# Kernel tuning notes

Hardware: AMD Instinct MI355X
Metric: run time of the kernel (lower is better)

## Reference

```python
import jax, jax.numpy as jnp
import numpy as np

N_NODES = 32768
N_EDGES = 65536
NODE_IN = 4
EDGE_IN = 4
HIDDEN = 64
LN_EPS = 1e-5


def setup_inputs() -> dict:
    key = jax.random.key(0)
    ks = jax.random.split(key, 20)
    s = 0.05
    inp = {
        "x": jax.random.normal(ks[0], (N_NODES, NODE_IN), dtype=jnp.float32),
        "edge_attr": jax.random.normal(ks[1], (N_EDGES, EDGE_IN), dtype=jnp.float32),
        "edge_index": jax.random.randint(ks[2], (2, N_EDGES), 0, N_NODES, dtype=jnp.int64),
        "batch": jnp.zeros((N_NODES,), dtype=jnp.int64),
        # layer 1: edge MLP edge_in->64->node_in*hidden, root [node_in,hidden]
        "e1_w1": jax.random.normal(ks[3], (EDGE_IN, 64), dtype=jnp.float32) * s,
        "e1_b1": jnp.zeros((64,), jnp.float32),
        "e1_w2": jax.random.normal(ks[4], (64, NODE_IN * HIDDEN), dtype=jnp.float32) * s,
        "e1_b2": jnp.zeros((NODE_IN * HIDDEN,), jnp.float32),
        "root1": jax.random.normal(ks[5], (NODE_IN, HIDDEN), dtype=jnp.float32) * s,
        "bias1": jnp.zeros((HIDDEN,), jnp.float32),
        "ln1_g": jnp.ones((HIDDEN,), jnp.float32),
        "ln1_b": jnp.zeros((HIDDEN,), jnp.float32),
        # layer 2: edge MLP edge_in->128->hidden*hidden, root [hidden,hidden]
        "e2_w1": jax.random.normal(ks[6], (EDGE_IN, 128), dtype=jnp.float32) * s,
        "e2_b1": jnp.zeros((128,), jnp.float32),
        "e2_w2": jax.random.normal(ks[7], (128, HIDDEN * HIDDEN), dtype=jnp.float32) * s,
        "e2_b2": jnp.zeros((HIDDEN * HIDDEN,), jnp.float32),
        "root2": jax.random.normal(ks[8], (HIDDEN, HIDDEN), dtype=jnp.float32) * s,
        "bias2": jnp.zeros((HIDDEN,), jnp.float32),
        "ln2_g": jnp.ones((HIDDEN,), jnp.float32),
        "ln2_b": jnp.zeros((HIDDEN,), jnp.float32),
    }
    return inp


def _nnconv(x, src, dst, edge_attr, ew1, eb1, ew2, eb2, root, bias, n_nodes):
    # edge-conditioned weights: [E, in_ch, out_ch]
    in_ch = x.shape[1]
    out_ch = root.shape[1]
    h = jax.nn.relu(edge_attr @ ew1 + eb1) @ ew2 + eb2
    W = h.reshape(-1, in_ch, out_ch)
    # gather source features, per-edge matvec, scatter-mean to dest
    msg = jnp.einsum('ei,eio->eo', x[src], W)  # [E, out_ch]
    summed = jax.ops.segment_sum(msg, dst, num_segments=n_nodes)
    cnt = jax.ops.segment_sum(jnp.ones((dst.shape[0],), msg.dtype), dst,
                              num_segments=n_nodes)
    agg = summed / jnp.maximum(cnt, 1.0)[:, None]
    return agg + x @ root + bias


def _layernorm(x, g, b):
    m = x.mean(-1, keepdims=True)
    v = ((x - m) ** 2).mean(-1, keepdims=True)
    return (x - m) * jax.lax.rsqrt(v + LN_EPS) * g + b


def reference(x, edge_attr, e1_w1, e1_b1, e1_w2, e1_b2, root1, bias1, ln1_g, ln1_b,
              e2_w1, e2_b1, e2_w2, e2_b2, root2, bias2, ln2_g, ln2_b,
              edge_index, batch):
    src, dst = edge_index[0], edge_index[1]
    n = x.shape[0]
    h = _nnconv(x, src, dst, edge_attr, e1_w1, e1_b1, e1_w2, e1_b2, root1, bias1, n)
    h = _layernorm(jax.nn.relu(h), ln1_g, ln1_b)  # dropout = identity (eval)
    h = _nnconv(h, src, dst, edge_attr, e2_w1, e2_b1, e2_w2, e2_b2, root2, bias2, n)
    h = _layernorm(jax.nn.relu(h), ln2_g, ln2_b)
    # global mean pool (single graph -> [1, hidden])
    gs = jax.ops.segment_sum(h, batch, num_segments=1)
    gc = jax.ops.segment_sum(jnp.ones((n,), h.dtype), batch, num_segments=1)
    return gs / jnp.maximum(gc, 1.0)[:, None]
```

## Files before the change

kernel.cpp:

```cpp
#include <hip/hip_runtime.h>

#define N_NODES 32768
#define N_EDGES 65536

typedef float f32x4 __attribute__((ext_vector_type(4)));
typedef short s16x8 __attribute__((ext_vector_type(8)));

__device__ __forceinline__ unsigned short f2bf(float f){
  unsigned u = __float_as_uint(f);
  u += 0x7FFFu + ((u >> 16) & 1u);
  return (unsigned short)(u >> 16);
}
__device__ __forceinline__ float bf2f(unsigned short b){
  return __uint_as_float(((unsigned)b) << 16);
}

__global__ void k_zero(int* __restrict__ p, int n){
  int i = blockIdx.x * 256 + threadIdx.x;
  if (i < n) p[i] = 0;
}

__global__ void k_prep(const float* __restrict__ e2_w2, const float* __restrict__ e2_b2,
                       const float* __restrict__ e1_w2,
                       unsigned short* __restrict__ W2f, unsigned short* __restrict__ T1g){
  int idx = blockIdx.x * 256 + threadIdx.x;
  if (idx < 129 * 4096){
    int j = idx & 7, l = (idx >> 3) & 63, half = (idx >> 9) & 1, ot = (idx >> 10) & 3, kf = idx >> 12;
    int i = half * 32 + ((l >> 4) << 3) + j;
    int o = ot * 16 + (l & 15);
    float v = (kf < 128) ? e2_w2[kf * 4096 + i * 64 + o] : e2_b2[i * 64 + o];
    W2f[idx] = f2bf(v);
  } else if (idx < 129 * 4096 + 16384){
    int t = idx - 129 * 4096;
    int j = t & 7, l = (t >> 3) & 63, half = (t >> 9) & 1, ot = (t >> 10) & 3, i = t >> 12;
    int kf = half * 32 + ((l >> 4) << 3) + j;
    int o = ot * 16 + (l & 15);
    T1g[t] = f2bf(e1_w2[kf * 256 + i * 64 + o]);
  }
}

__global__ void k_hist(const int* __restrict__ ei, int* __restrict__ cnti){
  int i = blockIdx.x * 256 + threadIdx.x;
  if (i < N_EDGES) atomicAdd(cnti + ei[N_EDGES + i], 1);
}

__global__ void k_scanA(const int* __restrict__ cnti, int* __restrict__ lex, int* __restrict__ bsum){
  const int tid = threadIdx.x;
  int n = blockIdx.x * 256 + tid;
  int c = cnti[n];
  int v = c;
  int lane = tid & 63;
  #pragma unroll
  for (int d = 1; d < 64; d <<= 1){
    int t = __shfl_up(v, d);
    if (lane >= d) v += t;
  }
  __shared__ int wsum[4];
  if (lane == 63) wsum[tid >> 6] = v;
  __syncthreads();
  int off = 0;
  for (int i = 0; i < (tid >> 6); ++i) off += wsum[i];
  lex[n] = off + v - c;
  if (tid == 255) bsum[blockIdx.x] = off + v;
}

__global__ void k_scanB(const int* __restrict__ bsum, int* __restrict__ bsx){
  const int tid = threadIdx.x;
  int c = bsum[tid];
  int v = c;
  int lane = tid & 63;
  #pragma unroll
  for (int d = 1; d < 64; d <<= 1){
    int t = __shfl_up(v, d);
    if (lane >= d) v += t;
  }
  __shared__ int w0;
  if (tid == 63) w0 = v;
  __syncthreads();
  if (tid >= 64) v += w0;
  bsx[tid] = v - c;
}

__global__ void k_fill(const int* __restrict__ ei, const int* __restrict__ lex,
                       const int* __restrict__ bsx, int* __restrict__ cur,
                       int* __restrict__ eslot){
  int e = blockIdx.x * 256 + threadIdx.x;
  if (e < N_EDGES){
    int d = ei[N_EDGES + e];
    int base = lex[d] + bsx[d >> 8];
    eslot[e] = base + atomicAdd(cur + d, 1);
  }
}

__launch_bounds__(256, 4)
__global__ void k_msg1(const float* __restrict__ x, const float* __restrict__ ea,
                       const int* __restrict__ ei, const int* __restrict__ eslot,
                       const float* __restrict__ e1_w1, const float* __restrict__ e1_b1,
                       const float* __restrict__ e1_b2,
                       const unsigned short* __restrict__ T1g,
                       float* __restrict__ msg)
{
  __shared__ float eas[64 * 4];
  __shared__ unsigned short F1f[8 * 64 * 8];
  const int tid = threadIdx.x;
  const int eblk = blockIdx.x * 64;

  if (tid < 64) ((float4*)eas)[tid] = ((const float4*)ea)[eblk + tid];
  __syncthreads();
  {
    int kf = tid & 63, eh = tid >> 6;
    float w0 = e1_w1[kf], w1 = e1_w1[64 + kf], w2 = e1_w1[128 + kf], w3 = e1_w1[192 + kf];
    float bb = e1_b1[kf];
    int half = kf >> 5, hi = (kf >> 3) & 3, j = kf & 7;
    for (int e = eh * 16; e < eh * 16 + 16; ++e){
      float s = fmaf(eas[e*4+0], w0, fmaf(eas[e*4+1], w1, fmaf(eas[e*4+2], w2, fmaf(eas[e*4+3], w3, bb))));
      F1f[(((e >> 4) * 2 + half) * 64 + hi * 16 + (e & 15)) * 8 + j] = f2bf(fmaxf(s, 0.f));
    }
  }
  __syncthreads();

  const int l = tid & 63, lm = l & 15, lg = l >> 4;
  const int ot = tid >> 6;
  int esl[4];
  float xs[4][4];
  s16x8 bf[4][2];
  #pragma unroll
  for (int et = 0; et < 4; ++et){
    int e = eblk + et * 16 + lm;
    int s = ei[e];
    esl[et] = eslot[e];
    float4 xv = *(const float4*)(x + s * 4);
    xs[et][0] = xv.x; xs[et][1] = xv.y; xs[et][2] = xv.z; xs[et][3] = xv.w;
    bf[et][0] = ((const s16x8*)F1f)[(et * 2 + 0) * 64 + l];
    bf[et][1] = ((const s16x8*)F1f)[(et * 2 + 1) * 64 + l];
  }
  f32x4 acc[4];
  #pragma unroll
  for (int et = 0; et < 4; ++et) acc[et] = (f32x4){0.f, 0.f, 0.f, 0.f};

  #pragma unroll
  for (int i = 0; i < 4; ++i){
    const s16x8* p = (const s16x8*)(T1g + (i * 4 + ot) * 1024);
    s16x8 a0 = p[l], a1 = p[64 + l];
    #pragma unroll
    for (int et = 0; et < 4; ++et){
      f32x4 g = (f32x4){0.f, 0.f, 0.f, 0.f};
      g = __builtin_amdgcn_mfma_f32_16x16x32_bf16(a0, bf[et][0], g, 0, 0, 0);
      g = __builtin_amdgcn_mfma_f32_16x16x32_bf16(a1, bf[et][1], g, 0, 0, 0);
      acc[et] += xs[et][i] * g;
    }
  }
  float b2v[4][4];
  #pragma unroll
  for (int i = 0; i < 4; ++i)
    #pragma unroll
    for (int r = 0; r < 4; ++r) b2v[i][r] = e1_b2[i * 64 + ot * 16 + lg * 4 + r];
  #pragma unroll
  for (int et = 0; et < 4; ++et)
    #pragma unroll
    for (int r = 0; r < 4; ++r)
      #pragma unroll
      for (int i = 0; i < 4; ++i) acc[et][r] = fmaf(xs[et][i], b2v[i][r], acc[et][r]);

  #pragma unroll
  for (int et = 0; et < 4; ++et)
    *(f32x4*)(msg + (size_t)esl[et] * 64 + ot * 16 + lg * 4) = acc[et];
}

__launch_bounds__(256)
__global__ void k_node1(const float* __restrict__ x, const float* __restrict__ root1,
                        const float* __restrict__ bias1, const float* __restrict__ lng,
                        const float* __restrict__ lnb, const int* __restrict__ cnti,
                        const int* __restrict__ lex, const int* __restrict__ bsx,
                        const float* __restrict__ msg, unsigned short* __restrict__ h1b)
{
  const int tid = threadIdx.x;
  int n = blockIdx.x * 4 + (tid >> 6);
  int o = tid & 63;
  int rp = lex[n] + bsx[n >> 8];
  int deg = cnti[n];
  float s = 0.f;
  for (int j = 0; j < deg; ++j) s += msg[(size_t)(rp + j) * 64 + o];
  float v = s * (1.f / fmaxf((float)deg, 1.f));
  float4 xv = *(const float4*)(x + n * 4);
  v = fmaf(xv.x, root1[o], v);
  v = fmaf(xv.y, root1[64 + o], v);
  v = fmaf(xv.z, root1[128 + o], v);
  v = fmaf(xv.w, root1[192 + o], v);
  v = fmaxf(v + bias1[o], 0.f);
  float m = v;
  #pragma unroll
  for (int d = 32; d > 0; d >>= 1) m += __shfl_xor(m, d);
  m *= (1.f / 64.f);
  float dd = v - m;
  float var = dd * dd;
  #pragma unroll
  for (int d = 32; d > 0; d >>= 1) var += __shfl_xor(var, d);
  var *= (1.f / 64.f);
  float out = dd * rsqrtf(var + 1e-5f) * lng[o] + lnb[o];
  h1b[n * 64 + o] = f2bf(out);
}

__launch_bounds__(512, 4)
__global__ void k_msg2(const float* __restrict__ ea, const int* __restrict__ ei,
                       const int* __restrict__ eslot,
                       const float* __restrict__ e2_w1, const float* __restrict__ e2_b1,
                       const unsigned short* __restrict__ h1b,
                       const unsigned short* __restrict__ W2f,
                       float* __restrict__ msg)
{
  __shared__ float eas[128 * 4];
  __shared__ float F2s[128 * 132];
  const int tid = threadIdx.x;
  const int eblk = blockIdx.x * 128;
  if (tid < 128) ((float4*)eas)[tid] = ((const float4*)ea)[eblk + tid];
  __syncthreads();
  {
    int kf = tid & 127, q = tid >> 7;
    float w0 = e2_w1[kf], w1 = e2_w1[128 + kf], w2 = e2_w1[256 + kf], w3 = e2_w1[384 + kf];
    float bb = e2_b1[kf];
    for (int e = q * 32; e < q * 32 + 32; ++e){
      float s = fmaf(eas[e*4+0], w0, fmaf(eas[e*4+1], w1, fmaf(eas[e*4+2], w2, fmaf(eas[e*4+3], w3, bb))));
      F2s[e * 132 + kf] = fmaxf(s, 0.f);
    }
  }
  __syncthreads();

  const int w = tid >> 6, l = tid & 63, lm = l & 15, lg = l >> 4;
  const int ot = w >> 1, eh = w & 1;
  int f2base[4], esl[4];
  s16x8 bh[4][2];
  #pragma unroll
  for (int et = 0; et < 4; ++et){
    int eloc = eh * 64 + et * 16 + lm;
    int e = eblk + eloc;
    int s = ei[e];
    esl[et] = eslot[e];
    f2base[et] = eloc * 132;
    const s16x8* hp = (const s16x8*)(h1b + s * 64);
    bh[et][0] = hp[lg];
    bh[et][1] = hp[4 + lg];
  }
  f32x4 acc[4];
  #pragma unroll
  for (int et = 0; et < 4; ++et) acc[et] = (f32x4){0.f, 0.f, 0.f, 0.f};

  const unsigned short* wbase = W2f + ot * 1024;
  s16x8 A0[2], A1[2], A2[2], A3[2];
  #define LOADA(DST, KF) { const s16x8* p = (const s16x8*)(wbase + (size_t)(KF) * 4096); DST[0] = p[l]; DST[1] = p[64 + l]; }
  #define STEP(A, J) { \
    _Pragma("unroll") \
    for (int et = 0; et < 4; ++et){ \
      float f2v = f2c[et][J]; \
      f32x4 g = (f32x4){0.f, 0.f, 0.f, 0.f}; \
      g = __builtin_amdgcn_mfma_f32_16x16x32_bf16(A[0], bh[et][0], g, 0, 0, 0); \
      g = __builtin_amdgcn_mfma_f32_16x16x32_bf16(A[1], bh[et][1], g, 0, 0, 0); \
      acc[et] += f2v * g; \
    } }

  LOADA(A0, 0)
  LOADA(A1, 1)
  #pragma unroll 1
  for (int ch = 0; ch < 32; ++ch){
    f32x4 f2c[4];
    #pragma unroll
    for (int et = 0; et < 4; ++et) f2c[et] = *(const f32x4*)&F2s[f2base[et] + ch * 4];
    const int kf = ch * 4;
    LOADA(A2, kf + 2)
    STEP(A0, 0)
    LOADA(A3, kf + 3)
    STEP(A1, 1)
    LOADA(A0, kf + 4)
    STEP(A2, 2)
    const int k5 = (kf + 5 > 128) ? 128 : kf + 5;
    LOADA(A1, k5)
    STEP(A3, 3)
  }
  #pragma unroll
  for (int et = 0; et < 4; ++et){
    acc[et] = __builtin_amdgcn_mfma_f32_16x16x32_bf16(A0[0], bh[et][0], acc[et], 0, 0, 0);
    acc[et] = __builtin_amdgcn_mfma_f32_16x16x32_bf16(A0[1], bh[et][1], acc[et], 0, 0, 0);
  }
  #undef LOADA
  #undef STEP

  #pragma unroll
  for (int et = 0; et < 4; ++et)
    *(f32x4*)(msg + (size_t)esl[et] * 64 + ot * 16 + lg * 4) = acc[et];
}

__launch_bounds__(1024)
__global__ void k_node2(const unsigned short* __restrict__ h1b, const float* __restrict__ root2,
                        const float* __restrict__ bias2, const float* __restrict__ lng,
                        const float* __restrict__ lnb, const int* __restrict__ cnti,
                        const int* __restrict__ lex, const int* __restrict__ bsx,
                        const float* __restrict__ msg, float* __restrict__ partial)
{
  const int tid = threadIdx.x;
  int n = blockIdx.x * 16 + (tid >> 6);
  int o = tid & 63;
  int rp = lex[n] + bsx[n >> 8];
  int deg = cnti[n];
  float s = 0.f;
  for (int j = 0; j < deg; ++j) s += msg[(size_t)(rp + j) * 64 + o];
  float v = s * (1.f / fmaxf((float)deg, 1.f));
  const s16x8* hp = (const s16x8*)(h1b + n * 64);
  #pragma unroll
  for (int c = 0; c < 8; ++c){
    s16x8 hv = hp[c];
    #pragma unroll
    for (int j = 0; j < 8; ++j)
      v = fmaf(bf2f((unsigned short)hv[j]), root2[(c * 8 + j) * 64 + o], v);
  }
  v = fmaxf(v + bias2[o], 0.f);
  float m = v;
  #pragma unroll
  for (int d = 32; d > 0; d >>= 1) m += __shfl_xor(m, d);
  m *= (1.f / 64.f);
  float dd = v - m;
  float var = dd * dd;
  #pragma unroll
  for (int d = 32; d > 0; d >>= 1) var += __shfl_xor(var, d);
  var *= (1.f / 64.f);
  float out = dd * rsqrtf(var + 1e-5f) * lng[o] + lnb[o];
  __shared__ float pp[16][64];
  pp[tid >> 6][o] = out;
  __syncthreads();
  if (tid < 64){
    float t = 0.f;
    #pragma unroll
    for (int k = 0; k < 16; ++k) t += pp[k][tid];
    partial[blockIdx.x * 64 + tid] = t;
  }
}

__launch_bounds__(1024)
__global__ void k_out(const float* __restrict__ partial, float* __restrict__ out){
  const int tid = threadIdx.x;
  int o = tid & 63, q = tid >> 6;
  float s = 0.f;
  for (int b = q; b < 2048; b += 16) s += partial[b * 64 + o];
  __shared__ float pp[16][64];
  pp[q][o] = s;
  __syncthreads();
  if (tid < 64){
    float t = 0.f;
    #pragma unroll
    for (int k = 0; k < 16; ++k) t += pp[k][tid];
    out[tid] = t * (1.f / 32768.f);
  }
}

extern "C" void kernel_launch(void* const* d_in, const int* in_sizes, int n_in,
                              void* d_out, int out_size, void* d_ws, size_t ws_size,
                              hipStream_t stream)
{
  const float* x      = (const float*)d_in[0];
  const float* ea     = (const float*)d_in[1];
  const int*   ei     = (const int*)  d_in[2];
  const float* e1_w1  = (const float*)d_in[4];
  const float* e1_b1  = (const float*)d_in[5];
  const float* e1_w2  = (const float*)d_in[6];
  const float* e1_b2  = (const float*)d_in[7];
  const float* root1  = (const float*)d_in[8];
  const float* bias1  = (const float*)d_in[9];
  const float* ln1g   = (const float*)d_in[10];
  const float* ln1b   = (const float*)d_in[11];
  const float* e2_w1  = (const float*)d_in[12];
  const float* e2_b1  = (const float*)d_in[13];
  const float* e2_w2  = (const float*)d_in[14];
  const float* e2_b2  = (const float*)d_in[15];
  const float* root2  = (const float*)d_in[16];
  const float* bias2  = (const float*)d_in[17];
  const float* ln2g   = (const float*)d_in[18];
  const float* ln2b   = (const float*)d_in[19];

  char* w = (char*)d_ws;
  float*          msg     = (float*)(w);
  unsigned short* h1b     = (unsigned short*)(w + 16777216);
  unsigned short* W2f     = (unsigned short*)(w + 20971520);
  unsigned short* T1g     = (unsigned short*)(w + 22028288);
  int*            cnti    = (int*)(w + 22061056);
  int*            cur     = (int*)(w + 22192128);
  int*            lex     = (int*)(w + 22323200);
  int*            bsx     = (int*)(w + 22454272);
  int*            bsum    = (int*)(w + 22454784);
  int*            eslot   = (int*)(w + 22455296);
  float*          partial = (float*)(w + 22717440);

  k_zero <<<256, 256, 0, stream>>>(cnti, 65536);
  k_prep <<<2128, 256, 0, stream>>>(e2_w2, e2_b2, e1_w2, W2f, T1g);
  k_hist <<<256, 256, 0, stream>>>(ei, cnti);
  k_scanA<<<128, 256, 0, stream>>>(cnti, lex, bsum);
  k_scanB<<<1, 128, 0, stream>>>(bsum, bsx);
  k_fill <<<256, 256, 0, stream>>>(ei, lex, bsx, cur, eslot);
  k_msg1 <<<1024, 256, 0, stream>>>(x, ea, ei, eslot, e1_w1, e1_b1, e1_b2, T1g, msg);
  k_node1<<<8192, 256, 0, stream>>>(x, root1, bias1, ln1g, ln1b, cnti, lex, bsx, msg, h1b);
  k_msg2 <<<512, 512, 0, stream>>>(ea, ei, eslot, e2_w1, e2_b1, h1b, W2f, msg);
  k_node2<<<2048, 1024, 0, stream>>>(h1b, root2, bias2, ln2g, ln2b, cnti, lex, bsx, msg, partial);
  k_out  <<<1, 1024, 0, stream>>>(partial, (float*)d_out);
}
```

Baseline: 175.9 us.

## Deepen msg2 weight prefetch with inline asm, fuse zeroing, batch node2 nodes

Folds the count-zeroing kernel into k_prep so there is one fewer launch. In k_msg2 the h1 gather is hoisted above the F2 edge-MLP stage so its latency overlaps that work. The weight loads become inline-asm global loads with explicit vmcnt waits, keeping four k-slices in flight instead of two. k_node2 now handles 64 nodes per block, so fewer partials go to k_out. Hand-written waitcnt and asm loads are fragile and may bypass compiler scheduling or raise register pressure.

```diff
diff --git a/kernel.cpp b/kernel.cpp
--- a/kernel.cpp
+++ b/kernel.cpp
@@ -15,14 +15,10 @@
   return __uint_as_float(((unsigned)b) << 16);
 }
 
-__global__ void k_zero(int* __restrict__ p, int n){
-  int i = blockIdx.x * 256 + threadIdx.x;
-  if (i < n) p[i] = 0;
-}
-
 __global__ void k_prep(const float* __restrict__ e2_w2, const float* __restrict__ e2_b2,
                        const float* __restrict__ e1_w2,
-                       unsigned short* __restrict__ W2f, unsigned short* __restrict__ T1g){
+                       unsigned short* __restrict__ W2f, unsigned short* __restrict__ T1g,
+                       int* __restrict__ cz){
   int idx = blockIdx.x * 256 + threadIdx.x;
   if (idx < 129 * 4096){
     int j = idx & 7, l = (idx >> 3) & 63, half = (idx >> 9) & 1, ot = (idx >> 10) & 3, kf = idx >> 12;
@@ -36,6 +32,9 @@
     int kf = half * 32 + ((l >> 4) << 3) + j;
     int o = ot * 16 + (l & 15);
     T1g[t] = f2bf(e1_w2[kf * 256 + i * 64 + o]);
+  } else {
+    int z = idx - (129 * 4096 + 16384);
+    if (z < 65536) cz[z] = 0;
   }
 }
 
@@ -213,6 +212,22 @@
   __shared__ float F2s[128 * 132];
   const int tid = threadIdx.x;
   const int eblk = blockIdx.x * 128;
+  const int w = tid >> 6, l = tid & 63, lm = l & 15, lg = l >> 4;
+  const int ot = w >> 1, eh = w & 1;
+
+  int esl[4];
+  s16x8 bh[4][2];
+  #pragma unroll
+  for (int et = 0; et < 4; ++et){
+    int eloc = eh * 64 + et * 16 + lm;
+    int e = eblk + eloc;
+    int s = ei[e];
+    esl[et] = eslot[e];
+    const s16x8* hp = (const s16x8*)(h1b + s * 64);
+    bh[et][0] = hp[lg];
+    bh[et][1] = hp[4 + lg];
+  }
+
   if (tid < 128) ((float4*)eas)[tid] = ((const float4*)ea)[eblk + tid];
   __syncthreads();
   {
@@ -226,63 +241,56 @@
   }
   __syncthreads();
 
-  const int w = tid >> 6, l = tid & 63, lm = l & 15, lg = l >> 4;
-  const int ot = w >> 1, eh = w & 1;
-  int f2base[4], esl[4];
-  s16x8 bh[4][2];
-  #pragma unroll
-  for (int et = 0; et < 4; ++et){
-    int eloc = eh * 64 + et * 16 + lm;
-    int e = eblk + eloc;
-    int s = ei[e];
-    esl[et] = eslot[e];
-    f2base[et] = eloc * 132;
-    const s16x8* hp = (const s16x8*)(h1b + s * 64);
-    bh[et][0] = hp[lg];
-    bh[et][1] = hp[4 + lg];
-  }
   f32x4 acc[4];
   #pragma unroll
   for (int et = 0; et < 4; ++et) acc[et] = (f32x4){0.f, 0.f, 0.f, 0.f};
 
-  const unsigned short* wbase = W2f + ot * 1024;
+  const int voff = ot * 2048 + l * 16;
   s16x8 A0[2], A1[2], A2[2], A3[2];
-  #define LOADA(DST, KF) { const s16x8* p = (const s16x8*)(wbase + (size_t)(KF) * 4096); DST[0] = p[l]; DST[1] = p[64 + l]; }
-  #define STEP(A, J) { \
+
+#define LOADA(DST, KF) { \
+    const unsigned short* sb = W2f + (size_t)(KF) * 4096; \
+    asm volatile("global_load_dwordx4 %0, %2, %3\n\t" \
+                 "global_load_dwordx4 %1, %2, %3 offset:1024" \
+      : "=&v"(DST[0]), "=&v"(DST[1]) : "v"(voff), "s"(sb)); }
+#define WAITA(N) do { asm volatile("s_waitcnt vmcnt(" #N ")"); \
+                      __builtin_amdgcn_sched_barrier(0); } while(0);
+#define STEP(A, J) { \
     _Pragma("unroll") \
     for (int et = 0; et < 4; ++et){ \
-      float f2v = f2c[et][J]; \
       f32x4 g = (f32x4){0.f, 0.f, 0.f, 0.f}; \
       g = __builtin_amdgcn_mfma_f32_16x16x32_bf16(A[0], bh[et][0], g, 0, 0, 0); \
       g = __builtin_amdgcn_mfma_f32_16x16x32_bf16(A[1], bh[et][1], g, 0, 0, 0); \
-      acc[et] += f2v * g; \
+      acc[et] += f2c[et][J] * g; \
     } }
 
   LOADA(A0, 0)
   LOADA(A1, 1)
+  LOADA(A2, 2)
+  LOADA(A3, 3)
   #pragma unroll 1
-  for (int ch = 0; ch < 32; ++ch){
+  for (int kf = 0; kf < 128; kf += 4){
     f32x4 f2c[4];
     #pragma unroll
-    for (int et = 0; et < 4; ++et) f2c[et] = *(const f32x4*)&F2s[f2base[et] + ch * 4];
-    const int kf = ch * 4;
-    LOADA(A2, kf + 2)
-    STEP(A0, 0)
-    LOADA(A3, kf + 3)
-    STEP(A1, 1)
-    LOADA(A0, kf + 4)
-    STEP(A2, 2)
+    for (int et = 0; et < 4; ++et)
+      f2c[et] = *(const f32x4*)&F2s[(eh * 64 + et * 16 + lm) * 132 + kf];
     const int k5 = (kf + 5 > 128) ? 128 : kf + 5;
-    LOADA(A1, k5)
-    STEP(A3, 3)
-  }
+    const int k6 = (kf + 6 > 128) ? 128 : kf + 6;
+    const int k7 = (kf + 7 > 128) ? 128 : kf + 7;
+    WAITA(6) STEP(A0, 0) LOADA(A0, kf + 4)
+    WAITA(6) STEP(A1, 1) LOADA(A1, k5)
+    WAITA(6) STEP(A2, 2) LOADA(A2, k6)
+    WAITA(6) STEP(A3, 3) LOADA(A3, k7)
+  }
+  WAITA(0)
   #pragma unroll
   for (int et = 0; et < 4; ++et){
     acc[et] = __builtin_amdgcn_mfma_f32_16x16x32_bf16(A0[0], bh[et][0], acc[et], 0, 0, 0);
     acc[et] = __builtin_amdgcn_mfma_f32_16x16x32_bf16(A0[1], bh[et][1], acc[et], 0, 0, 0);
   }
-  #undef LOADA
-  #undef STEP
+#undef LOADA
+#undef WAITA
+#undef STEP
 
   #pragma unroll
   for (int et = 0; et < 4; ++et)
@@ -297,34 +305,38 @@
                         const float* __restrict__ msg, float* __restrict__ partial)
 {
   const int tid = threadIdx.x;
-  int n = blockIdx.x * 16 + (tid >> 6);
-  int o = tid & 63;
-  int rp = lex[n] + bsx[n >> 8];
-  int deg = cnti[n];
-  float s = 0.f;
-  for (int j = 0; j < deg; ++j) s += msg[(size_t)(rp + j) * 64 + o];
-  float v = s * (1.f / fmaxf((float)deg, 1.f));
-  const s16x8* hp = (const s16x8*)(h1b + n * 64);
-  #pragma unroll
-  for (int c = 0; c < 8; ++c){
-    s16x8 hv = hp[c];
-    #pragma unroll
-    for (int j = 0; j < 8; ++j)
-      v = fmaf(bf2f((unsigned short)hv[j]), root2[(c * 8 + j) * 64 + o], v);
-  }
-  v = fmaxf(v + bias2[o], 0.f);
-  float m = v;
-  #pragma unroll
-  for (int d = 32; d > 0; d >>= 1) m += __shfl_xor(m, d);
-  m *= (1.f / 64.f);
-  float dd = v - m;
-  float var = dd * dd;
-  #pragma unroll
-  for (int d = 32; d > 0; d >>= 1) var += __shfl_xor(var, d);
-  var *= (1.f / 64.f);
-  float out = dd * rsqrtf(var + 1e-5f) * lng[o] + lnb[o];
+  const int q = tid >> 6, o = tid & 63;
+  float tsum = 0.f;
+  #pragma unroll 1
+  for (int it = 0; it < 4; ++it){
+    int n = blockIdx.x * 64 + it * 16 + q;
+    int rp = lex[n] + bsx[n >> 8];
+    int deg = cnti[n];
+    float s = 0.f;
+    for (int j = 0; j < deg; ++j) s += msg[(size_t)(rp + j) * 64 + o];
+    float v = s * (1.f / fmaxf((float)deg, 1.f));
+    const s16x8* hp = (const s16x8*)(h1b + n * 64);
+    #pragma unroll
+    for (int c = 0; c < 8; ++c){
+      s16x8 hv = hp[c];
+      #pragma unroll
+      for (int j = 0; j < 8; ++j)
+        v = fmaf(bf2f((unsigned short)hv[j]), root2[(c * 8 + j) * 64 + o], v);
+    }
+    v = fmaxf(v + bias2[o], 0.f);
+    float m = v;
+    #pragma unroll
+    for (int d = 32; d > 0; d >>= 1) m += __shfl_xor(m, d);
+    m *= (1.f / 64.f);
+    float dd = v - m;
+    float var = dd * dd;
+    #pragma unroll
+    for (int d = 32; d > 0; d >>= 1) var += __shfl_xor(var, d);
+    var *= (1.f / 64.f);
+    tsum += dd * rsqrtf(var + 1e-5f) * lng[o] + lnb[o];
+  }
   __shared__ float pp[16][64];
-  pp[tid >> 6][o] = out;
+  pp[q][o] = tsum;
   __syncthreads();
   if (tid < 64){
     float t = 0.f;
@@ -339,7 +351,7 @@
   const int tid = threadIdx.x;
   int o = tid & 63, q = tid >> 6;
   float s = 0.f;
-  for (int b = q; b < 2048; b += 16) s += partial[b * 64 + o];
+  for (int b = q; b < 512; b += 16) s += partial[b * 64 + o];
   __shared__ float pp[16][64];
   pp[q][o] = s;
   __syncthreads();
@@ -388,8 +400,7 @@
   int*            eslot   = (int*)(w + 22455296);
   float*          partial = (float*)(w + 22717440);
 
-  k_zero <<<256, 256, 0, stream>>>(cnti, 65536);
-  k_prep <<<2128, 256, 0, stream>>>(e2_w2, e2_b2, e1_w2, W2f, T1g);
+  k_prep <<<2384, 256, 0, stream>>>(e2_w2, e2_b2, e1_w2, W2f, T1g, cnti);
   k_hist <<<256, 256, 0, stream>>>(ei, cnti);
   k_scanA<<<128, 256, 0, stream>>>(cnti, lex, bsum);
   k_scanB<<<1, 128, 0, stream>>>(bsum, bsx);
@@ -397,6 +408,6 @@
   k_msg1 <<<1024, 256, 0, stream>>>(x, ea, ei, eslot, e1_w1, e1_b1, e1_b2, T1g, msg);
   k_node1<<<8192, 256, 0, stream>>>(x, root1, bias1, ln1g, ln1b, cnti, lex, bsx, msg, h1b);
   k_msg2 <<<512, 512, 0, stream>>>(ea, ei, eslot, e2_w1, e2_b1, h1b, W2f, msg);
-  k_node2<<<2048, 1024, 0, stream>>>(h1b, root2, bias2, ln2g, ln2b, cnti, lex, bsx, msg, partial);
+  k_node2<<<512, 1024, 0, stream>>>(h1b, root2, bias2, ln2g, ln2b, cnti, lex, bsx, msg, partial);
   k_out  <<<1, 1024, 0, stream>>>(partial, (float*)d_out);
 }
```

Measured after the change: 156.0 us, median of 2. -11.3%, faster.
